# Performance work log

Measured on AMD Instinct MI355X. Metric: run time of the kernel, lower is better.

Reference implementation:

```python
import jax, jax.numpy as jnp
import numpy as np

B, C, H, W = 8, 256, 64, 64
C8 = C // 8


def setup_inputs() -> dict:
    key = jax.random.key(0)
    ks = jax.random.split(key, 8)
    scale = 0.05
    return {
        "x": jax.random.normal(ks[0], (B, C, H, W), jnp.float32),
        "Wf": jax.random.normal(ks[1], (C8, C), jnp.float32) * scale,
        "bf": jax.random.normal(ks[2], (C8,), jnp.float32) * scale,
        "Wg": jax.random.normal(ks[3], (C8, C), jnp.float32) * scale,
        "bg": jax.random.normal(ks[4], (C8,), jnp.float32) * scale,
        "Wh": jax.random.normal(ks[5], (C, C), jnp.float32) * scale,
        "bh": jax.random.normal(ks[6], (C,), jnp.float32) * scale,
        "gamma": jax.random.normal(ks[7], (1,), jnp.float32) * scale,
    }


def reference(x, Wf, bf, Wg, bg, Wh, bh, gamma):
    b, c, h, w = x.shape
    n = h * w
    xr = x.reshape(b, c, n)  # flatten spatial: [B, C, N]
    # 1x1 convs == per-pixel linear projections
    f = jnp.einsum('oc,bcn->bon', Wf, xr) + bf[None, :, None]  # [B, C/8, N]
    g = jnp.einsum('oc,bcn->bon', Wg, xr) + bg[None, :, None]  # [B, C/8, N]
    hh = jnp.einsum('oc,bcn->bon', Wh, xr) + bh[None, :, None]  # [B, C, N]
    # s = f^T @ g : unscaled attention logits, [B, N, N]
    s = jnp.einsum('bki,bkj->bij', f, g)
    attention = jax.nn.softmax(s, axis=-1)
    # out = h @ attention^T : out[b,c,i] = sum_j h[b,c,j] * attn[b,i,j]
    out = jnp.einsum('bcj,bij->bci', hh, attention)
    out = out.reshape(b, c, w, h)  # original code uses (W, H); H==W here
    out = gamma[0] * out + x
    return (out, attention)
```

## Files before the change

kernel.cpp:

```cpp
#include <hip/hip_runtime.h>
#include <hip/hip_bf16.h>

typedef unsigned short u16;
typedef __attribute__((ext_vector_type(8))) short short8;
typedef __attribute__((ext_vector_type(4))) float f32x4;

#define BATCH 8
#define CH 256
#define NPIX 4096
#define KD 32

static __device__ __forceinline__ u16 f2bf(float f) {
  union { __hip_bfloat16 h; u16 u; } cv;
  cv.h = __float2bfloat16(f);
  return cv.u;
}

__global__ __launch_bounds__(256) void proj_kernel(
    const float* __restrict__ x,
    const float* __restrict__ Wf, const float* __restrict__ bfp,
    const float* __restrict__ Wg, const float* __restrict__ bgp,
    const float* __restrict__ Wh, const float* __restrict__ bhp,
    u16* __restrict__ fT, u16* __restrict__ gT, u16* __restrict__ hhb)
{
  __shared__ float xs[CH][36];
  const int b  = blockIdx.x >> 7;
  const int n0 = (blockIdx.x & 127) * 32;
  const int t  = threadIdx.x;

  const float* xb = x + ((size_t)b * CH) * NPIX + n0;
  #pragma unroll
  for (int kk = 0; kk < 8; ++kk) {
    int v = kk * 256 + t;
    int c = v >> 3, p4 = v & 7;
    float4 d = *(const float4*)(xb + (size_t)c * NPIX + p4 * 4);
    *(float4*)&xs[c][p4 * 4] = d;
  }
  __syncthreads();

  const int o = t;
  float acch[32];
  #pragma unroll
  for (int p = 0; p < 32; ++p) acch[p] = bhp[o];

  const int o2 = t & 63;
  const int oo = o2 & 31;
  const bool isf = o2 < 32;
  const float* Wfg = isf ? Wf : Wg;
  const float bias2 = isf ? bfp[oo] : bgp[oo];
  const int pg = (t >> 6) * 8;
  float accf[8];
  #pragma unroll
  for (int p = 0; p < 8; ++p) accf[p] = bias2;

  const float* whr  = Wh  + o * CH;
  const float* wfgr = Wfg + oo * CH;
  for (int c = 0; c < CH; c += 4) {
    float4 wh4 = *(const float4*)(whr + c);
    float4 wf4 = *(const float4*)(wfgr + c);
    float wha[4] = {wh4.x, wh4.y, wh4.z, wh4.w};
    float wfa[4] = {wf4.x, wf4.y, wf4.z, wf4.w};
    #pragma unroll
    for (int cc = 0; cc < 4; ++cc) {
      float wh = wha[cc], wf = wfa[cc];
      #pragma unroll
      for (int p4 = 0; p4 < 8; ++p4) {
        float4 xv = *(const float4*)&xs[c + cc][p4 * 4];
        acch[p4*4+0] = fmaf(wh, xv.x, acch[p4*4+0]);
        acch[p4*4+1] = fmaf(wh, xv.y, acch[p4*4+1]);
        acch[p4*4+2] = fmaf(wh, xv.z, acch[p4*4+2]);
        acch[p4*4+3] = fmaf(wh, xv.w, acch[p4*4+3]);
      }
      #pragma unroll
      for (int p = 0; p < 8; ++p) accf[p] = fmaf(wf, xs[c + cc][pg + p], accf[p]);
    }
  }

  u16* hrow = hhb + ((size_t)b * CH + o) * NPIX + n0;
  #pragma unroll
  for (int q = 0; q < 4; ++q) {
    uint4 u;
    u.x = f2bf(acch[q*8+0]) | ((unsigned)f2bf(acch[q*8+1]) << 16);
    u.y = f2bf(acch[q*8+2]) | ((unsigned)f2bf(acch[q*8+3]) << 16);
    u.z = f2bf(acch[q*8+4]) | ((unsigned)f2bf(acch[q*8+5]) << 16);
    u.w = f2bf(acch[q*8+6]) | ((unsigned)f2bf(acch[q*8+7]) << 16);
    *(uint4*)(hrow + q * 8) = u;
  }
  u16* dst = (isf ? fT : gT) + ((size_t)b * NPIX + n0 + pg) * KD + oo;
  #pragma unroll
  for (int p = 0; p < 8; ++p) dst[(size_t)p * KD] = f2bf(accf[p]);
}

__global__ __launch_bounds__(512, 4) void fused_attn_pv(
    const u16* __restrict__ fT, const u16* __restrict__ gT,
    const u16* __restrict__ hhb, const float* __restrict__ x,
    const float* __restrict__ gamma,
    float* __restrict__ attn_out, float* __restrict__ outp)
{
  __shared__ u16 Pt[2][64 * 32];
  __shared__ float part[8][64];
  __shared__ float invs[64];

  const int bid = blockIdx.x;
  const int b  = bid & 7;
  const int n0 = (bid >> 3) * 64;
  const int t  = threadIdx.x;
  const int iw = t >> 6, l = t & 63;
  const int lg = l >> 4, lm = l & 15;

  const u16* fb = fT + ((size_t)b * NPIX + n0) * KD;
  const u16* gb = gT + (size_t)b * NPIX * KD;
  const u16* hb = hhb + (size_t)b * CH * NPIX;

  f32x4 z4 = {0.f, 0.f, 0.f, 0.f};

  short8 ff[4];
  #pragma unroll
  for (int it = 0; it < 4; ++it)
    ff[it] = *(const short8*)(fb + (it * 16 + lm) * KD + lg * 8);

  float sum[4][4];
  #pragma unroll
  for (int it = 0; it < 4; ++it)
    #pragma unroll
    for (int r = 0; r < 4; ++r) sum[it][r] = 0.f;

  const int j1 = iw * 512;
  for (int jt = 0; jt < 32; ++jt) {
    int j0 = j1 + jt * 16;
    short8 gf = *(const short8*)(gb + (size_t)(j0 + lm) * KD + lg * 8);
    #pragma unroll
    for (int it = 0; it < 4; ++it) {
      f32x4 s = __builtin_amdgcn_mfma_f32_16x16x32_bf16(ff[it], gf, z4, 0, 0, 0);
      #pragma unroll
      for (int r = 0; r < 4; ++r) sum[it][r] += __expf(s[r]);
    }
  }
  #pragma unroll
  for (int m = 1; m < 16; m <<= 1)
    #pragma unroll
    for (int it = 0; it < 4; ++it)
      #pragma unroll
      for (int r = 0; r < 4; ++r) sum[it][r] += __shfl_xor(sum[it][r], m, 64);
  if (lm == 0) {
    #pragma unroll
    for (int it = 0; it < 4; ++it)
      #pragma unroll
      for (int r = 0; r < 4; ++r) part[iw][it * 16 + lg * 4 + r] = sum[it][r];
  }
  __syncthreads();
  if (t < 64) {
    float s = 0.f;
    #pragma unroll
    for (int w2 = 0; w2 < 8; ++w2) s += part[w2][t];
    invs[t] = 1.0f / s;
  }
  __syncthreads();

  const int it2 = iw >> 1, jsub = iw & 1;
  float inv4[4];
  #pragma unroll
  for (int r = 0; r < 4; ++r) inv4[r] = invs[it2 * 16 + lg * 4 + r];
  const short8 f2 = ff[it2];

  float* arow = attn_out + ((size_t)b * NPIX + n0 + it2 * 16 + lg * 4) * NPIX;
  const int rslot = ((lg ^ ((lm >> 1) & 3)) * 16);

  f32x4 acc[2][4];
  #pragma unroll
  for (int mf = 0; mf < 2; ++mf)
    #pragma unroll
    for (int nf = 0; nf < 4; ++nf) acc[mf][nf] = z4;

  auto chunk = [&](u16* bufp, int JC) {
    const int j0 = JC + jsub * 16;
    short8 gf = *(const short8*)(gb + (size_t)(j0 + lm) * KD + lg * 8);
    f32x4 s = __builtin_amdgcn_mfma_f32_16x16x32_bf16(f2, gf, z4, 0, 0, 0);
    #pragma unroll
    for (int r = 0; r < 4; ++r) {
      float p = __expf(s[r]) * inv4[r];
      arow[(size_t)r * NPIX + j0 + lm] = p;
      int iloc = it2 * 16 + lg * 4 + r;
      int jloc = jsub * 16 + lm;
      int byte = iloc * 64 + ((jloc * 2) ^ (((iloc >> 1) & 3) << 4));
      *(u16*)((char*)bufp + byte) = f2bf(p);
    }
    asm volatile("s_waitcnt lgkmcnt(0)\n\ts_barrier" ::: "memory");
    short8 af0 = *(const short8*)(hb + (size_t)(iw * 32 + lm) * NPIX + JC + lg * 8);
    short8 af1 = *(const short8*)(hb + (size_t)(iw * 32 + 16 + lm) * NPIX + JC + lg * 8);
    #pragma unroll
    for (int nf = 0; nf < 4; ++nf) {
      short8 bf8 = *(const short8*)((char*)bufp + (nf * 16 + lm) * 64 + rslot);
      acc[0][nf] = __builtin_amdgcn_mfma_f32_16x16x32_bf16(af0, bf8, acc[0][nf], 0, 0, 0);
      acc[1][nf] = __builtin_amdgcn_mfma_f32_16x16x32_bf16(af1, bf8, acc[1][nf], 0, 0, 0);
    }
  };

  for (int jc = 0; jc < NPIX; jc += 64) {
    chunk(&Pt[0][0], jc);
    chunk(&Pt[1][0], jc + 32);
  }

  const float gm = gamma[0];
  #pragma unroll
  for (int mf = 0; mf < 2; ++mf) {
    #pragma unroll
    for (int r = 0; r < 4; ++r) {
      int c = iw * 32 + mf * 16 + lg * 4 + r;
      #pragma unroll
      for (int nf = 0; nf < 4; ++nf) {
        int i = n0 + nf * 16 + lm;
        size_t idx = ((size_t)b * CH + c) * NPIX + i;
        outp[idx] = fmaf(gm, acc[mf][nf][r], x[idx]);
      }
    }
  }
}

extern "C" void kernel_launch(void* const* d_in, const int* in_sizes, int n_in,
                              void* d_out, int out_size, void* d_ws, size_t ws_size,
                              hipStream_t stream) {
  const float* x     = (const float*)d_in[0];
  const float* Wf    = (const float*)d_in[1];
  const float* bf    = (const float*)d_in[2];
  const float* Wg    = (const float*)d_in[3];
  const float* bg    = (const float*)d_in[4];
  const float* Wh    = (const float*)d_in[5];
  const float* bh    = (const float*)d_in[6];
  const float* gamma = (const float*)d_in[7];

  float* outp = (float*)d_out;
  float* attn_out = outp + (size_t)BATCH * CH * NPIX;

  u16* fT = (u16*)d_ws;
  u16* gT = fT + (size_t)BATCH * NPIX * KD;
  u16* hh = gT + (size_t)BATCH * NPIX * KD;

  proj_kernel<<<dim3(BATCH * (NPIX / 32)), dim3(256), 0, stream>>>(
      x, Wf, bf, Wg, bg, Wh, bh, fT, gT, hh);

  fused_attn_pv<<<dim3(BATCH * (NPIX / 64)), dim3(512), 0, stream>>>(
      fT, gT, hh, x, gamma, attn_out, outp);
}
```

Baseline: 388.1 us.

## Widen PV chunk to 64 columns and prefetch next g/h fragments

The PV loop now processes 64-column chunks per barrier instead of 32, which halves the number of barriers. Global loads of the next chunk's g and h fragments are issued in registers before the current chunk's softmax and MFMA work, using ping-pong register sets. The attention output is written with nontemporal stores and the LDS swizzle is redone for the wider tile. This raises register and LDS use, which may hurt occupancy under the 512x4 launch bounds, and the prefetch wraps around to index 0 on the last iteration.

```diff
diff --git a/kernel.cpp b/kernel.cpp
--- a/kernel.cpp
+++ b/kernel.cpp
@@ -97,7 +97,7 @@
     const float* __restrict__ gamma,
     float* __restrict__ attn_out, float* __restrict__ outp)
 {
-  __shared__ u16 Pt[2][64 * 32];
+  __shared__ u16 Pt[2][64 * 64];
   __shared__ float part[8][64];
   __shared__ float invs[64];
 
@@ -164,7 +164,6 @@
   const short8 f2 = ff[it2];
 
   float* arow = attn_out + ((size_t)b * NPIX + n0 + it2 * 16 + lg * 4) * NPIX;
-  const int rslot = ((lg ^ ((lm >> 1) & 3)) * 16);
 
   f32x4 acc[2][4];
   #pragma unroll
@@ -172,33 +171,59 @@
     #pragma unroll
     for (int nf = 0; nf < 4; ++nf) acc[mf][nf] = z4;
 
-  auto chunk = [&](u16* bufp, int JC) {
-    const int j0 = JC + jsub * 16;
-    short8 gf = *(const short8*)(gb + (size_t)(j0 + lm) * KD + lg * 8);
-    f32x4 s = __builtin_amdgcn_mfma_f32_16x16x32_bf16(f2, gf, z4, 0, 0, 0);
-    #pragma unroll
-    for (int r = 0; r < 4; ++r) {
-      float p = __expf(s[r]) * inv4[r];
-      arow[(size_t)r * NPIX + j0 + lm] = p;
-      int iloc = it2 * 16 + lg * 4 + r;
-      int jloc = jsub * 16 + lm;
-      int byte = iloc * 64 + ((jloc * 2) ^ (((iloc >> 1) & 3) << 4));
-      *(u16*)((char*)bufp + byte) = f2bf(p);
+  short8 gP[2], gQ[2], hP[2][2], hQ[2][2];
+
+  auto LDG = [&](short8 (&g2)[2], short8 (&h2)[2][2], int JC) {
+    #pragma unroll
+    for (int st = 0; st < 2; ++st)
+      g2[st] = *(const short8*)(gb + (size_t)(JC + jsub * 32 + st * 16 + lm) * KD + lg * 8);
+    #pragma unroll
+    for (int m = 0; m < 2; ++m)
+      #pragma unroll
+      for (int ks = 0; ks < 2; ++ks)
+        h2[m][ks] = *(const short8*)(hb + (size_t)(iw * 32 + m * 16 + lm) * NPIX
+                                     + JC + ks * 32 + lg * 8);
+  };
+
+  auto HALF = [&](u16* buf, short8 (&gc)[2], short8 (&hc)[2][2],
+                  short8 (&gn)[2], short8 (&hn)[2][2], int JC, int JN) {
+    f32x4 s[2];
+    #pragma unroll
+    for (int st = 0; st < 2; ++st)
+      s[st] = __builtin_amdgcn_mfma_f32_16x16x32_bf16(f2, gc[st], z4, 0, 0, 0);
+    LDG(gn, hn, JN);
+    #pragma unroll
+    for (int st = 0; st < 2; ++st) {
+      const int j0 = JC + jsub * 32 + st * 16;
+      #pragma unroll
+      for (int r = 0; r < 4; ++r) {
+        float p = __expf(s[st][r]) * inv4[r];
+        __builtin_nontemporal_store(p, arow + (size_t)r * NPIX + j0 + lm);
+        int iloc = it2 * 16 + lg * 4 + r;
+        int jloc = jsub * 32 + st * 16 + lm;
+        int byte = iloc * 128 + ((jloc * 2) ^ (((lg * 4 + r) & 7) << 4));
+        *(u16*)((char*)buf + byte) = f2bf(p);
+      }
     }
     asm volatile("s_waitcnt lgkmcnt(0)\n\ts_barrier" ::: "memory");
-    short8 af0 = *(const short8*)(hb + (size_t)(iw * 32 + lm) * NPIX + JC + lg * 8);
-    short8 af1 = *(const short8*)(hb + (size_t)(iw * 32 + 16 + lm) * NPIX + JC + lg * 8);
     #pragma unroll
     for (int nf = 0; nf < 4; ++nf) {
-      short8 bf8 = *(const short8*)((char*)bufp + (nf * 16 + lm) * 64 + rslot);
-      acc[0][nf] = __builtin_amdgcn_mfma_f32_16x16x32_bf16(af0, bf8, acc[0][nf], 0, 0, 0);
-      acc[1][nf] = __builtin_amdgcn_mfma_f32_16x16x32_bf16(af1, bf8, acc[1][nf], 0, 0, 0);
+      #pragma unroll
+      for (int ks = 0; ks < 2; ++ks) {
+        int byte = (nf * 16 + lm) * 128 + (((ks * 4 + lg) * 16) ^ ((lm & 7) << 4));
+        short8 pf = *(const short8*)((char*)buf + byte);
+        acc[0][nf] = __builtin_amdgcn_mfma_f32_16x16x32_bf16(hc[0][ks], pf, acc[0][nf], 0, 0, 0);
+        acc[1][nf] = __builtin_amdgcn_mfma_f32_16x16x32_bf16(hc[1][ks], pf, acc[1][nf], 0, 0, 0);
+      }
     }
   };
 
-  for (int jc = 0; jc < NPIX; jc += 64) {
-    chunk(&Pt[0][0], jc);
-    chunk(&Pt[1][0], jc + 32);
+  LDG(gP, hP, 0);
+  for (int jc = 0; jc < NPIX; jc += 128) {
+    int n1 = (jc + 64) & (NPIX - 1);
+    int n2 = (jc + 128) & (NPIX - 1);
+    HALF(&Pt[0][0], gP, hP, gQ, hQ, jc, n1);
+    HALF(&Pt[1][0], gQ, hQ, gP, hP, jc + 64, n2);
   }
 
   const float gm = gamma[0];
```

Measured after the change: 326.6 us. -15.8%, faster.
